# Kernel tuning notes

Hardware: AMD Instinct MI355X
Metric: run time of the kernel (lower is better)

## Reference

```python
import jax, jax.numpy as jnp
import numpy as np

BS, T, NOBJ = 16, 32, 100
GLOVE, GEMB, ADIM, GCN_DIM, H, ASPACE, RES = 300, 64, 10, 512, 512, 6, 512


def setup_inputs() -> dict:
    key = jax.random.key(0)
    ks = jax.random.split(key, 34)
    rn = lambda k, shp, s=0.02: (jax.random.normal(k, shp, jnp.float32) * s)
    inp = {}
    inp["target"] = jax.random.normal(ks[0], (BS, T, GLOVE), jnp.float32)
    inp["input_"] = jax.random.normal(ks[1], (BS, T, RES, 1, 1), jnp.float32)
    inp["action_probs"] = jax.random.uniform(ks[2], (BS, T, ASPACE), jnp.float32)
    # symmetric normalized adjacency (D^-1/2 A D^-1/2), as normalize_adj produces
    A_raw = (jax.random.uniform(ks[3], (NOBJ, NOBJ)) < 0.1).astype(jnp.float32)
    A_raw = ((A_raw + A_raw.T + jnp.eye(NOBJ)) > 0).astype(jnp.float32)
    dinv = 1.0 / jnp.sqrt(jnp.sum(A_raw, axis=1))
    inp["A"] = A_raw * dinv[:, None] * dinv[None, :]
    inp["all_glove"] = jax.random.normal(ks[4], (NOBJ, GLOVE), jnp.float32)
    inp["Wword"] = rn(ks[5], (GEMB, GLOVE)); inp["bword"] = jnp.zeros((GEMB,))
    inp["Wg"] = rn(ks[6], (GEMB, GLOVE)); inp["bg"] = jnp.zeros((GEMB,))
    inp["Wa"] = rn(ks[7], (ADIM, ASPACE)); inp["ba"] = jnp.zeros((ADIM,))
    inp["W0"] = rn(ks[8], (256, RES + GEMB))
    inp["W1"] = rn(ks[9], (256, 256))
    inp["W2"] = rn(ks[10], (1, 256))
    inp["Wfm"] = rn(ks[11], (GCN_DIM, NOBJ)); inp["bfm"] = jnp.zeros((GCN_DIM,))
    fused_in = RES + GEMB + ADIM + GCN_DIM
    inp["Wf"] = rn(ks[12], (H, fused_in)); inp["bf"] = jnp.zeros((H,))
    inp["Wih"] = rn(ks[13], (4 * H, H)); inp["Whh"] = rn(ks[14], (4 * H, H))
    inp["bih"] = jnp.zeros((4 * H,)); inp["bhh"] = jnp.zeros((4 * H,))
    inp["Wa1"] = rn(ks[15], (128, H)); inp["ba1"] = jnp.zeros((128,))
    inp["Wa2"] = rn(ks[16], (ASPACE, 128)); inp["ba2"] = jnp.zeros((ASPACE,))
    inp["Wc1"] = rn(ks[17], (128, H)); inp["bc1"] = jnp.zeros((128,))
    inp["Wc2"] = rn(ks[18], (1, 128)); inp["bc2"] = jnp.zeros((1,))
    return inp


def _forward(target, input_, action_probs, A, all_glove, Wword, bword, Wg, bg,
             Wa, ba, W0, W1, W2, Wfm, bfm, Wf, bf, Wih, Whh, bih, bhh,
             Wa1, ba1, Wa2, ba2, Wc1, bc1, Wc2, bc2):
    bs, t = target.shape[0], target.shape[1]
    B = bs * t
    feats = input_.reshape(B, RES)                      # [B,512] (squeeze 1x1)
    glove_e = jax.nn.relu(target.reshape(B, GLOVE) @ Wg.T + bg)
    act_e = jax.nn.relu(action_probs.reshape(B, ASPACE) @ Wa.T + ba)
    # GCN branch (all_glove is detached in the original)
    word = jax.lax.stop_gradient(all_glove) @ Wword.T + bword   # [N,GEMB]
    N = A.shape[0]
    class_e = jnp.broadcast_to(feats[:, None, :], (B, N, RES))
    x = jnp.concatenate([class_e, jnp.broadcast_to(word[None], (B, N, GEMB))], -1)
    x = jax.nn.relu(jnp.einsum('nm,bmd->bnd', A, x) @ W0.T)     # [B,N,256]
    x = jax.nn.relu(jnp.einsum('nm,bmd->bnd', A, x) @ W1.T)     # [B,N,256]
    x = jax.nn.relu(jnp.einsum('nm,bmd->bnd', A, x) @ W2.T)     # [B,N,1]
    gcn_e = x[..., 0] @ Wfm.T + bfm                             # [B,GCN_DIM]
    fused = jnp.concatenate([feats, glove_e, act_e, gcn_e], -1)
    out = jax.nn.relu(fused @ Wf.T + bf).reshape(bs, t, H)
    # LSTM (torch gate order i,f,g,o), batch_first, zero init state
    h0 = jnp.zeros((bs, H), out.dtype)
    c0 = jnp.zeros((bs, H), out.dtype)
    def step(carry, xt):
        h, c = carry
        g = xt @ Wih.T + h @ Whh.T + bih + bhh
        i, f, gg, o = jnp.split(g, 4, axis=-1)
        c = jax.nn.sigmoid(f) * c + jax.nn.sigmoid(i) * jnp.tanh(gg)
        h = jax.nn.sigmoid(o) * jnp.tanh(c)
        return (h, c), h
    (hT, cT), hs = jax.lax.scan(step, (h0, c0), out.transpose(1, 0, 2))
    sf = hs.transpose(1, 0, 2).reshape(B, H)
    actor = jax.nn.relu(jax.nn.relu(sf @ Wa1.T + ba1) @ Wa2.T + ba2).reshape(bs, t, ASPACE)
    critic = jax.nn.relu(jax.nn.relu(sf @ Wc1.T + bc1) @ Wc2.T + bc2).reshape(bs, t, 1)
    return actor, critic, hT[None], cT[None]


def reference(target, input_, action_probs, A, all_glove, Wword, bword, Wg, bg,
              Wa, ba, W0, W1, W2, Wfm, bfm, Wf, bf, Wih, Whh, bih, bhh,
              Wa1, ba1, Wa2, ba2, Wc1, bc1, Wc2, bc2):
    return _forward(target, input_, action_probs, A, all_glove, Wword, bword,
                    Wg, bg, Wa, ba, W0, W1, W2, Wfm, bfm, Wf, bf, Wih, Whh,
                    bih, bhh, Wa1, ba1, Wa2, ba2, Wc1, bc1, Wc2, bc2)
```

## Files before the change

kernel.cpp:

```cpp
#include <hip/hip_runtime.h>
#include <cmath>

constexpr int BSZ = 16, T = 32, NOBJ = 100;
constexpr int GLOVE = 300, GEMB = 64, ADIM = 10, GCN_DIM = 512, Hh = 512, ASPACE = 6, RES = 512;
constexpr int Bt = BSZ * T;
constexpr int FUSED_IN = RES + GEMB + ADIM + GCN_DIM;
constexpr int FP = 1120;

typedef __attribute__((ext_vector_type(8))) short bf16x8;
typedef __attribute__((ext_vector_type(4))) float f32x4;

__device__ __forceinline__ unsigned short f2bf(float f) {
    unsigned u = __float_as_uint(f);
    return (unsigned short)((u + 0x7FFFu + ((u >> 16) & 1u)) >> 16);
}
__device__ __forceinline__ unsigned pk2(float a, float b) {
    return (unsigned)f2bf(a) | ((unsigned)f2bf(b) << 16);
}
__device__ __forceinline__ float sigf(float x) { return 1.f / (1.f + __expf(-x)); }

template<bool RELU, int OMODE>
__global__ __launch_bounds__(256)
void mgemm(const unsigned short* __restrict__ A, int lda,
           const unsigned short* __restrict__ B, int ldb,
           float* __restrict__ Cf, unsigned short* __restrict__ Cb, int ldc,
           const float* __restrict__ bias, int K)
{
    const int tid = threadIdx.x;
    const int l = tid & 63, wv = tid >> 6;
    const int m0 = blockIdx.y * 64 + wv * 16;
    const int n0 = blockIdx.x * 64;
    const int lr = l & 15, kg = l >> 4;
    const unsigned short* ap = A + (long)(m0 + lr) * lda + kg * 8;
    const unsigned short* bp = B + (long)(n0 + lr) * ldb + kg * 8;
    const int nk = K >> 5;
    f32x4 acc0 = (f32x4){0.f, 0.f, 0.f, 0.f};
    f32x4 acc1 = acc0, acc2 = acc0, acc3 = acc0;
    bf16x8 a_[4], b0_[4], b1_[4], b2_[4], b3_[4];
#pragma unroll
    for (int s = 0; s < 4; ++s) {
        if (s < nk) {
            int k = s * 32;
            a_[s]  = *(const bf16x8*)(ap + k);
            b0_[s] = *(const bf16x8*)(bp + k);
            b1_[s] = *(const bf16x8*)(bp + 16 * ldb + k);
            b2_[s] = *(const bf16x8*)(bp + 32 * ldb + k);
            b3_[s] = *(const bf16x8*)(bp + 48 * ldb + k);
        }
    }
    for (int i = 0; i < nk; i += 4) {
#pragma unroll
        for (int s = 0; s < 4; ++s) {
            if (i + s < nk) {
                acc0 = __builtin_amdgcn_mfma_f32_16x16x32_bf16(a_[s], b0_[s], acc0, 0, 0, 0);
                acc1 = __builtin_amdgcn_mfma_f32_16x16x32_bf16(a_[s], b1_[s], acc1, 0, 0, 0);
                acc2 = __builtin_amdgcn_mfma_f32_16x16x32_bf16(a_[s], b2_[s], acc2, 0, 0, 0);
                acc3 = __builtin_amdgcn_mfma_f32_16x16x32_bf16(a_[s], b3_[s], acc3, 0, 0, 0);
                if (i + s + 4 < nk) {
                    int k = (i + s + 4) * 32;
                    a_[s]  = *(const bf16x8*)(ap + k);
                    b0_[s] = *(const bf16x8*)(bp + k);
                    b1_[s] = *(const bf16x8*)(bp + 16 * ldb + k);
                    b2_[s] = *(const bf16x8*)(bp + 32 * ldb + k);
                    b3_[s] = *(const bf16x8*)(bp + 48 * ldb + k);
                }
            }
        }
    }
    f32x4 av[4] = {acc0, acc1, acc2, acc3};
#pragma unroll
    for (int nf = 0; nf < 4; ++nf) {
        int n = n0 + nf * 16 + lr;
        float bs = bias ? bias[n] : 0.f;
#pragma unroll
        for (int r = 0; r < 4; ++r) {
            float val = av[nf][r] + bs;
            if (RELU) val = fmaxf(val, 0.f);
            long idx = (long)(m0 + kg * 4 + r) * ldc + n;
            if (OMODE == 0) Cf[idx] = val;
            else            Cb[idx] = f2bf(val);
        }
    }
}

template<bool RELU>
__global__ __launch_bounds__(128)
void gemm32(const float* __restrict__ A, int lda,
            const float* __restrict__ B, int ldb,
            float* __restrict__ C, int ldc,
            const float* __restrict__ bias, int M, int N, int K)
{
    __shared__ float As[32][36];
    __shared__ float Bs[32][68];
    const int tid = threadIdx.x;
    const int m0 = blockIdx.y * 32, n0 = blockIdx.x * 64;
    const int mi = tid >> 4, ni = tid & 15;
    float acc[4][4] = {};
    for (int k0 = 0; k0 < K; k0 += 32) {
        __syncthreads();
#pragma unroll
        for (int l = 0; l < 2; ++l) {
            int e = tid + l * 128;
            int row = e >> 3, kq = (e & 7) << 2;
            float4 va = make_float4(0.f, 0.f, 0.f, 0.f);
            if (m0 + row < M && k0 + kq < K)
                va = *(const float4*)&A[(long)(m0 + row) * lda + k0 + kq];
            As[kq + 0][row] = va.x; As[kq + 1][row] = va.y;
            As[kq + 2][row] = va.z; As[kq + 3][row] = va.w;
        }
#pragma unroll
        for (int l = 0; l < 4; ++l) {
            int e = tid + l * 128;
            int row = e >> 3, kq = (e & 7) << 2;
            float4 vb = make_float4(0.f, 0.f, 0.f, 0.f);
            if (n0 + row < N && k0 + kq < K)
                vb = *(const float4*)&B[(long)(n0 + row) * ldb + k0 + kq];
            Bs[kq + 0][row] = vb.x; Bs[kq + 1][row] = vb.y;
            Bs[kq + 2][row] = vb.z; Bs[kq + 3][row] = vb.w;
        }
        __syncthreads();
#pragma unroll
        for (int k = 0; k < 32; ++k) {
            float4 a4 = *(const float4*)&As[k][4 * mi];
            float4 b4 = *(const float4*)&Bs[k][4 * ni];
            acc[0][0] = fmaf(a4.x, b4.x, acc[0][0]); acc[0][1] = fmaf(a4.x, b4.y, acc[0][1]);
            acc[0][2] = fmaf(a4.x, b4.z, acc[0][2]); acc[0][3] = fmaf(a4.x, b4.w, acc[0][3]);
            acc[1][0] = fmaf(a4.y, b4.x, acc[1][0]); acc[1][1] = fmaf(a4.y, b4.y, acc[1][1]);
            acc[1][2] = fmaf(a4.y, b4.z, acc[1][2]); acc[1][3] = fmaf(a4.y, b4.w, acc[1][3]);
            acc[2][0] = fmaf(a4.z, b4.x, acc[2][0]); acc[2][1] = fmaf(a4.z, b4.y, acc[2][1]);
            acc[2][2] = fmaf(a4.z, b4.z, acc[2][2]); acc[2][3] = fmaf(a4.z, b4.w, acc[2][3]);
            acc[3][0] = fmaf(a4.w, b4.x, acc[3][0]); acc[3][1] = fmaf(a4.w, b4.y, acc[3][1]);
            acc[3][2] = fmaf(a4.w, b4.z, acc[3][2]); acc[3][3] = fmaf(a4.w, b4.w, acc[3][3]);
        }
    }
    const int n = n0 + 4 * ni;
    if (n >= N) return;
    float4 bv = make_float4(0.f, 0.f, 0.f, 0.f);
    if (bias) bv = *(const float4*)&bias[n];
#pragma unroll
    for (int r = 0; r < 4; ++r) {
        int m = m0 + 4 * mi + r;
        if (m >= M) continue;
        float4 v;
        v.x = acc[r][0] + bv.x; v.y = acc[r][1] + bv.y;
        v.z = acc[r][2] + bv.z; v.w = acc[r][3] + bv.w;
        if (RELU) {
            v.x = fmaxf(v.x, 0.f); v.y = fmaxf(v.y, 0.f);
            v.z = fmaxf(v.z, 0.f); v.w = fmaxf(v.w, 0.f);
        }
        *(float4*)&C[(long)m * ldc + n] = v;
    }
}

__global__ __launch_bounds__(256)
void x1pack(const float* __restrict__ u, const float* __restrict__ v,
            const float* __restrict__ rowsum, uint4* __restrict__ X1g)
{
    __shared__ float u_lds[256];
    __shared__ float rs_lds[112];
    const int b = blockIdx.x, tid = threadIdx.x;
    u_lds[tid] = u[(long)b * 256 + tid];
    if (tid < 112) rs_lds[tid] = (tid < 100) ? rowsum[tid] : 0.f;
    __syncthreads();
    uint4* outp = X1g + (size_t)b * 3584;
#pragma unroll
    for (int it = 0; it < 14; ++it) {
        int job = it * 256 + tid;
        int l = job & 63;
        int kt = (job >> 6) & 7;
        int mt = job >> 9;
        int n = mt * 16 + (l & 15);
        int k0 = kt * 32 + ((l >> 4) << 3);
        uint4 p = make_uint4(0, 0, 0, 0);
        if (n < 100) {
            float rsn = rs_lds[n];
            float4 u0 = *(const float4*)&u_lds[k0];
            float4 u1 = *(const float4*)&u_lds[k0 + 4];
            const float4* vp = (const float4*)&v[n * 256 + k0];
            float4 v0 = vp[0], v1 = vp[1];
            float x0 = fmaxf(fmaf(rsn, u0.x, v0.x), 0.f), x1 = fmaxf(fmaf(rsn, u0.y, v0.y), 0.f);
            float x2 = fmaxf(fmaf(rsn, u0.z, v0.z), 0.f), x3 = fmaxf(fmaf(rsn, u0.w, v0.w), 0.f);
            float x4 = fmaxf(fmaf(rsn, u1.x, v1.x), 0.f), x5 = fmaxf(fmaf(rsn, u1.y, v1.y), 0.f);
            float x6 = fmaxf(fmaf(rsn, u1.z, v1.z), 0.f), x7 = fmaxf(fmaf(rsn, u1.w, v1.w), 0.f);
            p = make_uint4(pk2(x0, x1), pk2(x2, x3), pk2(x4, x5), pk2(x6, x7));
        }
        outp[job] = p;
    }
}

constexpr int ZLD = 152;

__global__ __launch_bounds__(256, 2)
void gcn_core(const bf16x8* __restrict__ X1g,
              const float* __restrict__ Aglob,
              const bf16x8* __restrict__ W1f,
              const bf16x8* __restrict__ Af,
              const float* __restrict__ w2,
              unsigned short* __restrict__ x3b)
{
    __shared__ unsigned short Z1Ts[128 * ZLD];
    __shared__ float w2l[256];
    __shared__ float spart[4][112];
    __shared__ float sl[112];

    const int b = blockIdx.x, tid = threadIdx.x;
    const int l = tid & 63, wv = tid >> 6;
    const int lrow = l & 15, kg = l >> 4;

    w2l[tid] = w2[tid];
    if (tid < 128) {
        uint4 z = make_uint4(0, 0, 0, 0);
        *(uint4*)&Z1Ts[tid * ZLD + 112] = z;
        *(uint4*)&Z1Ts[tid * ZLD + 120] = z;
    }
    if (tid < 28) x3b[(long)b * 128 + 100 + tid] = 0;
    __syncthreads();

    const bf16x8* xb = X1g + (size_t)b * 3584 + l;

    float sacc[7][4];
#pragma unroll
    for (int mt = 0; mt < 7; ++mt)
#pragma unroll
        for (int r = 0; r < 4; ++r) sacc[mt][r] = 0.f;

    for (int half = 0; half < 2; ++half) {
        f32x4 acc1[7][2];
#pragma unroll
        for (int mt = 0; mt < 7; ++mt)
#pragma unroll
            for (int jtl = 0; jtl < 2; ++jtl) acc1[mt][jtl] = (f32x4){0.f, 0.f, 0.f, 0.f};

#pragma unroll
        for (int kt = 0; kt < 8; ++kt) {
            bf16x8 af[7];
#pragma unroll
            for (int mt = 0; mt < 7; ++mt)
                af[mt] = xb[mt * 512 + kt * 64];
#pragma unroll
            for (int jtl = 0; jtl < 2; ++jtl) {
                int jt = half * 8 + wv * 2 + jtl;
                bf16x8 bfr = W1f[(jt * 8 + kt) * 64 + l];
#pragma unroll
                for (int mt = 0; mt < 7; ++mt)
                    acc1[mt][jtl] = __builtin_amdgcn_mfma_f32_16x16x32_bf16(af[mt], bfr, acc1[mt][jtl], 0, 0, 0);
            }
        }

#pragma unroll
        for (int mt = 0; mt < 7; ++mt)
#pragma unroll
            for (int jtl = 0; jtl < 2; ++jtl) {
                int jloc = (wv * 2 + jtl) * 16 + lrow;
                f32x4 a = acc1[mt][jtl];
                uint2 zz;
                zz.x = pk2(a[0], a[1]);
                zz.y = pk2(a[2], a[3]);
                *(uint2*)&Z1Ts[jloc * ZLD + mt * 16 + kg * 4] = zz;
            }

        bf16x8 bz[2][4];
#pragma unroll
        for (int jtl = 0; jtl < 2; ++jtl)
#pragma unroll
            for (int k2 = 0; k2 < 4; ++k2)
                bz[jtl][k2] = *(const bf16x8*)&Z1Ts[((wv * 2 + jtl) * 16 + lrow) * ZLD + k2 * 32 + kg * 8];
#pragma unroll
        for (int mt = 0; mt < 7; ++mt) {
            bf16x8 aA[4];
#pragma unroll
            for (int k2 = 0; k2 < 4; ++k2) aA[k2] = Af[(mt * 4 + k2) * 64 + l];
#pragma unroll
            for (int jtl = 0; jtl < 2; ++jtl) {
                f32x4 p = (f32x4){0.f, 0.f, 0.f, 0.f};
#pragma unroll
                for (int k2 = 0; k2 < 4; ++k2)
                    p = __builtin_amdgcn_mfma_f32_16x16x32_bf16(aA[k2], bz[jtl][k2], p, 0, 0, 0);
                float w2j = w2l[half * 128 + (wv * 2 + jtl) * 16 + lrow];
#pragma unroll
                for (int r = 0; r < 4; ++r)
                    sacc[mt][r] = fmaf(fmaxf(p[r], 0.f), w2j, sacc[mt][r]);
            }
        }
    }

#pragma unroll
    for (int mt = 0; mt < 7; ++mt) {
        float s0 = sacc[mt][0], s1 = sacc[mt][1], s2 = sacc[mt][2], s3 = sacc[mt][3];
#pragma unroll
        for (int off = 1; off < 16; off <<= 1) {
            s0 += __shfl_xor(s0, off);
            s1 += __shfl_xor(s1, off);
            s2 += __shfl_xor(s2, off);
            s3 += __shfl_xor(s3, off);
        }
        if (lrow == 0) {
            int m = mt * 16 + kg * 4;
            spart[wv][m + 0] = s0; spart[wv][m + 1] = s1;
            spart[wv][m + 2] = s2; spart[wv][m + 3] = s3;
        }
    }
    __syncthreads();
    if (tid < 112)
        sl[tid] = spart[0][tid] + spart[1][tid] + spart[2][tid] + spart[3][tid];
    __syncthreads();

    float sv0 = (l < 100) ? sl[l] : 0.f;
    float sv1 = (l + 64 < 100) ? sl[l + 64] : 0.f;
#pragma unroll 5
    for (int i = 0; i < 25; ++i) {
        int n = i * 4 + wv;
        float a0 = (l < 100) ? Aglob[n * 100 + l] : 0.f;
        float a1 = (l + 64 < 100) ? Aglob[n * 100 + l + 64] : 0.f;
        float p = a0 * sv0 + a1 * sv1;
#pragma unroll
        for (int off = 32; off; off >>= 1) p += __shfl_xor(p, off);
        if (l == 0) x3b[(long)b * 128 + n] = f2bf(fmaxf(p, 0.f));
    }
}

union HU { unsigned long long u[2]; bf16x8 v; };

__global__ __launch_bounds__(256, 1)
void lstm_persist3(const float* __restrict__ xWih,
                   const bf16x8* __restrict__ Whhf,
                   unsigned long long* __restrict__ hseq,
                   unsigned* __restrict__ flags,
                   float* __restrict__ cBuf, float* __restrict__ hFin,
                   unsigned short* __restrict__ sfb)
{
    __shared__ float gl[4][16][17];
    __shared__ unsigned short htile[16][16];
    const int tid = threadIdx.x;
    const int l = tid & 63, g = tid >> 6;
    const int bid = blockIdx.x;
    const int jt = g * 32 + bid;
    const int lr = l & 15, kg = l >> 4;
    const bf16x8* wp = Whhf + (size_t)jt * 16 * 64 + l;
    bf16x8 w[16];
#pragma unroll
    for (int kt = 0; kt < 16; ++kt) w[kt] = wp[kt * 64];
    const int fb = tid >> 4, jl = tid & 15;
    const int jh = bid * 16 + jl;
    float c_reg = 0.f;
    for (int t = 0; t < T; ++t) {
        if (t > 0) {
            if (tid < 32) {
                while (__hip_atomic_load(&flags[t * 32 + tid],
                                         __ATOMIC_RELAXED, __HIP_MEMORY_SCOPE_AGENT) == 0u) { }
            }
            __syncthreads();
        }
        const unsigned long long* hp = hseq + (size_t)t * 2048 + lr * 128 + kg * 2;
        HU hu[16];
#pragma unroll
        for (int kt = 0; kt < 16; ++kt) {
            hu[kt].u[0] = __hip_atomic_load(hp + kt * 8,     __ATOMIC_RELAXED, __HIP_MEMORY_SCOPE_AGENT);
            hu[kt].u[1] = __hip_atomic_load(hp + kt * 8 + 1, __ATOMIC_RELAXED, __HIP_MEMORY_SCOPE_AGENT);
        }
        f32x4 acc = (f32x4){0.f, 0.f, 0.f, 0.f};
#pragma unroll
        for (int kt = 0; kt < 16; ++kt)
            acc = __builtin_amdgcn_mfma_f32_16x16x32_bf16(hu[kt].v, w[kt], acc, 0, 0, 0);
#pragma unroll
        for (int r = 0; r < 4; ++r) gl[g][kg * 4 + r][lr] = acc[r];
        __syncthreads();
        const float* xw = xWih + (size_t)(fb * T + t) * 2048;
        float gi = gl[0][fb][jl] + xw[jh];
        float gf = gl[1][fb][jl] + xw[512 + jh];
        float gg = gl[2][fb][jl] + xw[1024 + jh];
        float go = gl[3][fb][jl] + xw[1536 + jh];
        float cn = sigf(gf) * c_reg + sigf(gi) * tanhf(gg);
        float hn = sigf(go) * tanhf(cn);
        c_reg = cn;
        unsigned short hb = f2bf(hn);
        htile[fb][jl] = hb;
        sfb[(size_t)(fb * T + t) * 512 + jh] = hb;
        if (t == T - 1) { hFin[fb * 512 + jh] = hn; cBuf[fb * 512 + jh] = cn; }
        __syncthreads();
        if (tid < 64) {
            int row = tid >> 2, q = tid & 3;
            unsigned long long val = *(const unsigned long long*)&htile[row][q * 4];
            __hip_atomic_store(&hseq[(size_t)(t + 1) * 2048 + row * 128 + bid * 4 + q], val,
                               __ATOMIC_RELAXED, __HIP_MEMORY_SCOPE_AGENT);
        }
        __syncthreads();
        if (tid == 0)
            __hip_atomic_store(&flags[(t + 1) * 32 + bid], 1u,
                               __ATOMIC_RELAXED, __HIP_MEMORY_SCOPE_AGENT);
    }
}

__global__ void k_aw_rowsum(const float* __restrict__ A, const float* __restrict__ word,
                            float* __restrict__ Aw, float* __restrict__ rowsum)
{
    int i = blockIdx.x * 256 + threadIdx.x;
    if (i < 6400) {
        int n = i / 64, k = i % 64;
        float s = 0.f;
        for (int m = 0; m < 100; ++m) s += A[n * 100 + m] * word[m * 64 + k];
        Aw[i] = s;
    } else if (i < 6500) {
        int n = i - 6400;
        float s = 0.f;
        for (int m = 0; m < 100; ++m) s += A[n * 100 + m];
        rowsum[n] = s;
    }
}

__global__ void k_prep(const float* __restrict__ Whh, uint4* __restrict__ Whhf,
                       const float* __restrict__ Wf, unsigned short* __restrict__ WfPb,
                       const float* __restrict__ Wih, unsigned short* __restrict__ Wihb,
                       const float* __restrict__ Wa1, const float* __restrict__ Wc1,
                       unsigned short* __restrict__ Whdb,
                       const float* __restrict__ ba1, const float* __restrict__ bc1,
                       float* __restrict__ bhd,
                       const float* __restrict__ Wg, unsigned short* __restrict__ Wgb,
                       const float* __restrict__ W0, unsigned short* __restrict__ W0ab,
                       const float* __restrict__ Wfm, unsigned short* __restrict__ Wfmb,
                       const float* __restrict__ target, unsigned short* __restrict__ tgtb,
                       const float* __restrict__ feats, unsigned short* __restrict__ featsb,
                       unsigned short* __restrict__ fusedb,
                       const float* __restrict__ aprob, const float* __restrict__ Wa,
                       const float* __restrict__ ba,
                       unsigned short* __restrict__ h0s, unsigned* __restrict__ flags,
                       const float* __restrict__ bih, const float* __restrict__ bhh,
                       float* __restrict__ bsum,
                       const float* __restrict__ W1, uint4* __restrict__ W1f,
                       const float* __restrict__ A, uint4* __restrict__ Af)
{
    int bx = blockIdx.x, tid = threadIdx.x;
    if (bx < 512) {
        int job = bx * 256 + tid;
        int jtkt = job >> 6, ll = job & 63;
        int j = (jtkt >> 4) * 16 + (ll & 15);
        int k0 = (jtkt & 15) * 32 + (ll >> 4) * 8;
        const float* src = &Whh[(long)j * 512 + k0];
        uint4 p;
        p.x = pk2(src[0], src[1]); p.y = pk2(src[2], src[3]);
        p.z = pk2(src[4], src[5]); p.w = pk2(src[6], src[7]);
        Whhf[job] = p;
    } else if (bx < 2752) {
        int i = (bx - 512) * 256 + tid;
        int r = i / FP, c = i - r * FP;
        WfPb[i] = f2bf(c < FUSED_IN ? Wf[(long)r * FUSED_IN + c] : 0.f);
    } else if (bx < 6848) {
        int i = (bx - 2752) * 256 + tid;
        Wihb[i] = f2bf(Wih[i]);
    } else if (bx < 7360) {
        int i = (bx - 6848) * 256 + tid;
        int r = i >> 9, c = i & 511;
        Whdb[i] = f2bf(r < 128 ? Wa1[r * 512 + c] : Wc1[(r - 128) * 512 + c]);
    } else if (bx < 7361) {
        bhd[tid] = (tid < 128) ? ba1[tid] : bc1[tid - 128];
    } else if (bx < 7441) {
        int i = (bx - 7361) * 256 + tid;
        int r = i / 320, c = i - r * 320;
        Wgb[i] = f2bf(c < GLOVE ? Wg[r * GLOVE + c] : 0.f);
    } else if (bx < 7953) {
        int i = (bx - 7441) * 256 + tid;
        int r = i >> 9, c = i & 511;
        W0ab[i] = f2bf(W0[(long)r * 576 + c]);
    } else if (bx < 8209) {
        int i = (bx - 7953) * 256 + tid;
        int r = i >> 7, c = i & 127;
        Wfmb[i] = f2bf(c < 100 ? Wfm[r * 100 + c] : 0.f);
    } else if (bx < 8849) {
        int i = (bx - 8209) * 256 + tid;
        int r = i / 320, c = i - r * 320;
        tgtb[i] = f2bf(c < GLOVE ? target[(long)r * GLOVE + c] : 0.f);
    } else if (bx < 9873) {
        int i = (bx - 8849) * 256 + tid;
        featsb[i] = f2bf(feats[i]);
    } else if (bx < 10897) {
        int i = (bx - 9873) * 256 + tid;
        int r = i >> 9, c = i & 511;
        fusedb[(long)r * FP + c] = f2bf(feats[i]);
    } else if (bx < 10917) {
        int i = (bx - 10897) * 256 + tid;
        int r = i / 10, c6 = i - r * 10;
        float s = ba[c6];
#pragma unroll
        for (int k = 0; k < 6; ++k) s += aprob[r * 6 + k] * Wa[c6 * 6 + k];
        fusedb[(long)r * FP + 576 + c6] = f2bf(fmaxf(s, 0.f));
    } else if (bx < 10961) {
        int i = (bx - 10917) * 256 + tid;
        int r = i / 22, c = 1098 + (i - r * 22);
        fusedb[(long)r * FP + c] = 0;
    } else if (bx < 10993) {
        int i = (bx - 10961) * 256 + tid;
        h0s[i] = 0;
    } else if (bx < 10998) {
        int i = (bx - 10993) * 256 + tid;
        if (i < (T + 1) * 32) flags[i] = 0u;
    } else if (bx < 11006) {
        int i = (bx - 10998) * 256 + tid;
        bsum[i] = bih[i] + bhh[i];
    } else if (bx < 11038) {
        int job = (bx - 11006) * 256 + tid;
        int jt = job >> 9, rem = job & 511, kt = rem >> 6, lane = rem & 63;
        int j = jt * 16 + (lane & 15), k0 = kt * 32 + (lane >> 4) * 8;
        const float* src = &W1[(long)j * 256 + k0];
        uint4 p;
        p.x = pk2(src[0], src[1]); p.y = pk2(src[2], src[3]);
        p.z = pk2(src[4], src[5]); p.w = pk2(src[6], src[7]);
        W1f[job] = p;
    } else {
        int job = (bx - 11038) * 256 + tid;
        int mt = job >> 8, rem = job & 255, kt = rem >> 6, lane = rem & 63;
        int m = mt * 16 + (lane & 15), n0 = kt * 32 + (lane >> 4) * 8;
        float h[8];
#pragma unroll
        for (int e = 0; e < 8; ++e)
            h[e] = (m < 100 && n0 + e < 100) ? A[m * 100 + n0 + e] : 0.f;
        uint4 p;
        p.x = pk2(h[0], h[1]); p.y = pk2(h[2], h[3]);
        p.z = pk2(h[4], h[5]); p.w = pk2(h[6], h[7]);
        Af[job] = p;
    }
}

__global__ void k_finish(const float* __restrict__ hd,
                         const float* __restrict__ Wa2, const float* __restrict__ ba2,
                         const float* __restrict__ Wc2, const float* __restrict__ bc2,
                         const float* __restrict__ hFin, const float* __restrict__ cBuf,
                         float* __restrict__ out)
{
    if (blockIdx.x < 32) {
        int row = blockIdx.x * 16 + (threadIdx.x >> 4);
        int slot = threadIdx.x & 15;
        if (slot < 6) {
            const float4* h4 = (const float4*)(hd + (long)row * 256);
            const float4* w4 = (const float4*)(Wa2 + slot * 128);
            float s = 0.f;
#pragma unroll
            for (int k = 0; k < 32; ++k) {
                float4 h = h4[k], w = w4[k];
                s += h.x * w.x + h.y * w.y + h.z * w.z + h.w * w.w;
            }
            out[row * 6 + slot] = fmaxf(s + ba2[slot], 0.f);
        } else if (slot == 6) {
            const float4* h4 = (const float4*)(hd + (long)row * 256 + 128);
            const float4* w4 = (const float4*)(Wc2);
            float s = 0.f;
#pragma unroll
            for (int k = 0; k < 32; ++k) {
                float4 h = h4[k], w = w4[k];
                s += h.x * w.x + h.y * w.y + h.z * w.z + h.w * w.w;
            }
            out[3072 + row] = fmaxf(s + bc2[0], 0.f);
        }
    } else {
        int i = (blockIdx.x - 32) * 256 + threadIdx.x;
        out[3584 + i] = hFin[i];
        out[11776 + i] = cBuf[i];
    }
}

static inline void mg(hipStream_t st, const unsigned short* A, int lda,
                      const unsigned short* B, int ldb,
                      float* Cf, unsigned short* Cb, int ldc,
                      const float* bias, int M, int N, int K, bool relu, bool bf16out)
{
    dim3 g(N / 64, M / 64), blk(256);
    if (bf16out) {
        if (relu) hipLaunchKernelGGL((mgemm<true, 1>), g, blk, 0, st, A, lda, B, ldb, Cf, Cb, ldc, bias, K);
        else      hipLaunchKernelGGL((mgemm<false, 1>), g, blk, 0, st, A, lda, B, ldb, Cf, Cb, ldc, bias, K);
    } else {
        if (relu) hipLaunchKernelGGL((mgemm<true, 0>), g, blk, 0, st, A, lda, B, ldb, Cf, Cb, ldc, bias, K);
        else      hipLaunchKernelGGL((mgemm<false, 0>), g, blk, 0, st, A, lda, B, ldb, Cf, Cb, ldc, bias, K);
    }
}
static inline void g32(hipStream_t st, const float* A, int lda, const float* B, int ldb,
                       float* C, int ldc, const float* bias, int M, int N, int K, bool relu)
{
    dim3 g((N + 63) / 64, (M + 31) / 32), blk(128);
    if (relu) hipLaunchKernelGGL((gemm32<true>), g, blk, 0, st, A, lda, B, ldb, C, ldc, bias, M, N, K);
    else      hipLaunchKernelGGL((gemm32<false>), g, blk, 0, st, A, lda, B, ldb, C, ldc, bias, M, N, K);
}

extern "C" void kernel_launch(void* const* d_in, const int* in_sizes, int n_in,
                              void* d_out, int out_size, void* d_ws, size_t ws_size,
                              hipStream_t stream)
{
    const float* target = (const float*)d_in[0];
    const float* input_ = (const float*)d_in[1];
    const float* aprob  = (const float*)d_in[2];
    const float* Adj    = (const float*)d_in[3];
    const float* aglove = (const float*)d_in[4];
    const float* Wword  = (const float*)d_in[5];
    const float* bword  = (const float*)d_in[6];
    const float* Wg     = (const float*)d_in[7];
    const float* bg     = (const float*)d_in[8];
    const float* Wa     = (const float*)d_in[9];
    const float* ba     = (const float*)d_in[10];
    const float* W0     = (const float*)d_in[11];
    const float* W1     = (const float*)d_in[12];
    const float* W2     = (const float*)d_in[13];
    const float* Wfm    = (const float*)d_in[14];
    const float* bfm    = (const float*)d_in[15];
    const float* Wf     = (const float*)d_in[16];
    const float* bf     = (const float*)d_in[17];
    const float* Wih    = (const float*)d_in[18];
    const float* Whh    = (const float*)d_in[19];
    const float* bih    = (const float*)d_in[20];
    const float* bhh    = (const float*)d_in[21];
    const float* Wa1    = (const float*)d_in[22];
    const float* ba1    = (const float*)d_in[23];
    const float* Wa2    = (const float*)d_in[24];
    const float* ba2    = (const float*)d_in[25];
    const float* Wc1    = (const float*)d_in[26];
    const float* bc1    = (const float*)d_in[27];
    const float* Wc2    = (const float*)d_in[28];
    const float* bc2    = (const float*)d_in[29];

    float* ws = (float*)d_ws;
    float* out = (float*)d_out;

    size_t off = 0;
    auto alloc = [&](size_t n) { size_t r = off; off += (n + 255) & ~(size_t)255; return r; };
    float* u       = ws + alloc(512 * 256);
    float* word    = ws + alloc(100 * 64);
    float* Aw      = ws + alloc(100 * 64);
    float* rowsum  = ws + alloc(128);
    float* v       = ws + alloc(100 * 256);
    float* bsum    = ws + alloc(2048);
    float* bhd     = ws + alloc(256);
    float* xWih    = ws + alloc((size_t)512 * 2048);
    float* hd      = ws + alloc(512 * 256);
    float* hFin    = ws + alloc(BSZ * Hh);
    float* cBuf    = ws + alloc(BSZ * Hh);
    float* W1frag  = ws + alloc(32768);
    float* Afrag   = ws + alloc(7168);
    float* Whhf    = ws + alloc((size_t)524288);
    float* X1gf    = ws + alloc((size_t)512 * 3584 * 4);
    float* hseqf   = ws + alloc((size_t)(T + 1) * 2048 * 2);
    unsigned* flags = (unsigned*)(ws + alloc(2048));
    unsigned short* x3b     = (unsigned short*)(ws + alloc(512 * 128 / 2));
    unsigned short* fusedb  = (unsigned short*)(ws + alloc((size_t)512 * FP / 2));
    unsigned short* WfPb    = (unsigned short*)(ws + alloc((size_t)512 * FP / 2));
    unsigned short* outfb   = (unsigned short*)(ws + alloc(512 * 512 / 2));
    unsigned short* Wihb    = (unsigned short*)(ws + alloc((size_t)2048 * 512 / 2));
    unsigned short* Whdb    = (unsigned short*)(ws + alloc(256 * 512 / 2));
    unsigned short* Wgb     = (unsigned short*)(ws + alloc(64 * 320 / 2));
    unsigned short* W0ab    = (unsigned short*)(ws + alloc(256 * 512 / 2));
    unsigned short* Wfmb    = (unsigned short*)(ws + alloc(512 * 128 / 2));
    unsigned short* tgtb    = (unsigned short*)(ws + alloc(512 * 320 / 2));
    unsigned short* featsb  = (unsigned short*)(ws + alloc(512 * 512 / 2));
    unsigned short* sfb     = (unsigned short*)(ws + alloc(512 * 512 / 2));
    (void)ws_size; (void)in_sizes; (void)n_in; (void)out_size;

    const float* feats = input_;

    hipLaunchKernelGGL(k_prep, dim3(11045), dim3(256), 0, stream,
                       Whh, (uint4*)Whhf, Wf, WfPb, Wih, Wihb, Wa1, Wc1, Whdb, ba1, bc1, bhd,
                       Wg, Wgb, W0, W0ab, Wfm, Wfmb, target, tgtb, feats, featsb,
                       fusedb, aprob, Wa, ba,
                       (unsigned short*)hseqf, flags, bih, bhh, bsum,
                       W1, (uint4*)W1frag, Adj, (uint4*)Afrag);

    g32(stream, aglove, GLOVE, Wword, GLOVE, word, 64, bword, 100, 64, GLOVE, false);
    hipLaunchKernelGGL(k_aw_rowsum, dim3(26), dim3(256), 0, stream, Adj, word, Aw, rowsum);
    g32(stream, Aw, 64, W0 + 512, 576, v, 256, nullptr, 100, 256, 64, false);

    mg(stream, featsb, 512, W0ab, 512, u, nullptr, 256, nullptr, 512, 256, 512, false, false);
    mg(stream, tgtb, 320, Wgb, 320, nullptr, fusedb + 512, FP, bg, 512, 64, 320, true, true);

    hipLaunchKernelGGL(x1pack, dim3(Bt), dim3(256), 0, stream, u, v, rowsum, (uint4*)X1gf);
    hipLaunchKernelGGL(gcn_core, dim3(Bt), dim3(256), 0, stream,
                       (const bf16x8*)X1gf, Adj, (const bf16x8*)W1frag, (const bf16x8*)Afrag, W2, x3b);
    mg(stream, x3b, 128, Wfmb, 128, nullptr, fusedb + 586, FP, bfm, 512, 512, 128, false, true);

    mg(stream, fusedb, FP, WfPb, FP, nullptr, outfb, 512, bf, 512, 512, FP, true, true);
    mg(stream, outfb, 512, Wihb, 512, xWih, nullptr, 2048, bsum, 512, 2048, 512, false, false);

    hipLaunchKernelGGL(lstm_persist3, dim3(32), dim3(256), 0, stream,
                       xWih, (const bf16x8*)Whhf,
                       (unsigned long long*)hseqf, flags, cBuf, hFin, sfb);

    mg(stream, sfb, 512, Whdb, 512, hd, nullptr, 256, bhd, 512, 256, 512, true, false);
    hipLaunchKernelGGL(k_finish, dim3(64), dim3(256), 0, stream,
                       hd, Wa2, ba2, Wc2, bc2, hFin, cBuf, out);
}
```

Baseline: 377.0 us.

## Replace LSTM per-step flag barrier with data-embedded sentinel polling on hidden state

The persistent LSTM kernel no longer waits on per-block flags followed by a block barrier. Each thread now polls its own 64-bit hidden-state words directly until they become nonzero, using zero as a sentinel. A computed zero word is replaced by 1, which alters those bf16 values slightly. The prep kernel now zeroes the hidden-sequence buffer for steps 1 and later, and step 0 skips the recurrent matmul because h0 is zero. This removes the flag store, two syncthreads per step, and a serialized handshake, at the cost of more polling traffic.

```diff
diff --git a/kernel.cpp b/kernel.cpp
--- a/kernel.cpp
+++ b/kernel.cpp
@@ -322,10 +322,9 @@
 union HU { unsigned long long u[2]; bf16x8 v; };
 
 __global__ __launch_bounds__(256, 1)
-void lstm_persist3(const float* __restrict__ xWih,
+void lstm_persist4(const float* __restrict__ xWih,
                    const bf16x8* __restrict__ Whhf,
                    unsigned long long* __restrict__ hseq,
-                   unsigned* __restrict__ flags,
                    float* __restrict__ cBuf, float* __restrict__ hFin,
                    unsigned short* __restrict__ sfb)
 {
@@ -344,24 +343,29 @@
     const int jh = bid * 16 + jl;
     float c_reg = 0.f;
     for (int t = 0; t < T; ++t) {
+        f32x4 acc = (f32x4){0.f, 0.f, 0.f, 0.f};
         if (t > 0) {
-            if (tid < 32) {
-                while (__hip_atomic_load(&flags[t * 32 + tid],
-                                         __ATOMIC_RELAXED, __HIP_MEMORY_SCOPE_AGENT) == 0u) { }
-            }
-            __syncthreads();
-        }
-        const unsigned long long* hp = hseq + (size_t)t * 2048 + lr * 128 + kg * 2;
-        HU hu[16];
-#pragma unroll
-        for (int kt = 0; kt < 16; ++kt) {
-            hu[kt].u[0] = __hip_atomic_load(hp + kt * 8,     __ATOMIC_RELAXED, __HIP_MEMORY_SCOPE_AGENT);
-            hu[kt].u[1] = __hip_atomic_load(hp + kt * 8 + 1, __ATOMIC_RELAXED, __HIP_MEMORY_SCOPE_AGENT);
-        }
-        f32x4 acc = (f32x4){0.f, 0.f, 0.f, 0.f};
-#pragma unroll
-        for (int kt = 0; kt < 16; ++kt)
-            acc = __builtin_amdgcn_mfma_f32_16x16x32_bf16(hu[kt].v, w[kt], acc, 0, 0, 0);
+            const unsigned long long* hp = hseq + (size_t)t * 2048 + lr * 128 + kg * 2;
+            unsigned long long hv[32];
+#pragma unroll
+            for (int kt = 0; kt < 16; ++kt) {
+                hv[2 * kt]     = __hip_atomic_load(hp + kt * 8,     __ATOMIC_RELAXED, __HIP_MEMORY_SCOPE_AGENT);
+                hv[2 * kt + 1] = __hip_atomic_load(hp + kt * 8 + 1, __ATOMIC_RELAXED, __HIP_MEMORY_SCOPE_AGENT);
+            }
+#pragma unroll
+            for (int q = 0; q < 32; ++q) {
+                while (hv[q] == 0ull)
+                    hv[q] = __hip_atomic_load(hp + (q >> 1) * 8 + (q & 1),
+                                              __ATOMIC_RELAXED, __HIP_MEMORY_SCOPE_AGENT);
+            }
+#pragma unroll
+            for (int kt = 0; kt < 16; ++kt) {
+                HU hu;
+                hu.u[0] = hv[2 * kt];
+                hu.u[1] = hv[2 * kt + 1];
+                acc = __builtin_amdgcn_mfma_f32_16x16x32_bf16(hu.v, w[kt], acc, 0, 0, 0);
+            }
+        }
 #pragma unroll
         for (int r = 0; r < 4; ++r) gl[g][kg * 4 + r][lr] = acc[r];
         __syncthreads();
@@ -381,13 +385,10 @@
         if (tid < 64) {
             int row = tid >> 2, q = tid & 3;
             unsigned long long val = *(const unsigned long long*)&htile[row][q * 4];
+            if (val == 0ull) val = 1ull;
             __hip_atomic_store(&hseq[(size_t)(t + 1) * 2048 + row * 128 + bid * 4 + q], val,
                                __ATOMIC_RELAXED, __HIP_MEMORY_SCOPE_AGENT);
         }
-        __syncthreads();
-        if (tid == 0)
-            __hip_atomic_store(&flags[(t + 1) * 32 + bid], 1u,
-                               __ATOMIC_RELAXED, __HIP_MEMORY_SCOPE_AGENT);
     }
 }
 
@@ -423,7 +424,7 @@
                        unsigned short* __restrict__ fusedb,
                        const float* __restrict__ aprob, const float* __restrict__ Wa,
                        const float* __restrict__ ba,
-                       unsigned short* __restrict__ h0s, unsigned* __restrict__ flags,
+                       unsigned long long* __restrict__ hz,
                        const float* __restrict__ bih, const float* __restrict__ bhh,
                        float* __restrict__ bsum,
                        const float* __restrict__ W1, uint4* __restrict__ W1f,
@@ -487,17 +488,14 @@
         int i = (bx - 10917) * 256 + tid;
         int r = i / 22, c = 1098 + (i - r * 22);
         fusedb[(long)r * FP + c] = 0;
-    } else if (bx < 10993) {
+    } else if (bx < 11217) {
         int i = (bx - 10961) * 256 + tid;
-        h0s[i] = 0;
-    } else if (bx < 10998) {
-        int i = (bx - 10993) * 256 + tid;
-        if (i < (T + 1) * 32) flags[i] = 0u;
-    } else if (bx < 11006) {
-        int i = (bx - 10998) * 256 + tid;
+        __hip_atomic_store(&hz[2048 + i], 0ull, __ATOMIC_RELAXED, __HIP_MEMORY_SCOPE_AGENT);
+    } else if (bx < 11225) {
+        int i = (bx - 11217) * 256 + tid;
         bsum[i] = bih[i] + bhh[i];
-    } else if (bx < 11038) {
-        int job = (bx - 11006) * 256 + tid;
+    } else if (bx < 11257) {
+        int job = (bx - 11225) * 256 + tid;
         int jt = job >> 9, rem = job & 511, kt = rem >> 6, lane = rem & 63;
         int j = jt * 16 + (lane & 15), k0 = kt * 32 + (lane >> 4) * 8;
         const float* src = &W1[(long)j * 256 + k0];
@@ -506,7 +504,7 @@
         p.z = pk2(src[4], src[5]); p.w = pk2(src[6], src[7]);
         W1f[job] = p;
     } else {
-        int job = (bx - 11038) * 256 + tid;
+        int job = (bx - 11257) * 256 + tid;
         int mt = job >> 8, rem = job & 255, kt = rem >> 6, lane = rem & 63;
         int m = mt * 16 + (lane & 15), n0 = kt * 32 + (lane >> 4) * 8;
         float h[8];
@@ -635,7 +633,6 @@
     float* Whhf    = ws + alloc((size_t)524288);
     float* X1gf    = ws + alloc((size_t)512 * 3584 * 4);
     float* hseqf   = ws + alloc((size_t)(T + 1) * 2048 * 2);
-    unsigned* flags = (unsigned*)(ws + alloc(2048));
     unsigned short* x3b     = (unsigned short*)(ws + alloc(512 * 128 / 2));
     unsigned short* fusedb  = (unsigned short*)(ws + alloc((size_t)512 * FP / 2));
     unsigned short* WfPb    = (unsigned short*)(ws + alloc((size_t)512 * FP / 2));
@@ -652,11 +649,11 @@
 
     const float* feats = input_;
 
-    hipLaunchKernelGGL(k_prep, dim3(11045), dim3(256), 0, stream,
+    hipLaunchKernelGGL(k_prep, dim3(11264), dim3(256), 0, stream,
                        Whh, (uint4*)Whhf, Wf, WfPb, Wih, Wihb, Wa1, Wc1, Whdb, ba1, bc1, bhd,
                        Wg, Wgb, W0, W0ab, Wfm, Wfmb, target, tgtb, feats, featsb,
                        fusedb, aprob, Wa, ba,
-                       (unsigned short*)hseqf, flags, bih, bhh, bsum,
+                       (unsigned long long*)hseqf, bih, bhh, bsum,
                        W1, (uint4*)W1frag, Adj, (uint4*)Afrag);
 
     g32(stream, aglove, GLOVE, Wword, GLOVE, word, 64, bword, 100, 64, GLOVE, false);
@@ -674,9 +671,9 @@
     mg(stream, fusedb, FP, WfPb, FP, nullptr, outfb, 512, bf, 512, 512, FP, true, true);
     mg(stream, outfb, 512, Wihb, 512, xWih, nullptr, 2048, bsum, 512, 2048, 512, false, false);
 
-    hipLaunchKernelGGL(lstm_persist3, dim3(32), dim3(256), 0, stream,
+    hipLaunchKernelGGL(lstm_persist4, dim3(32), dim3(256), 0, stream,
                        xWih, (const bf16x8*)Whhf,
-                       (unsigned long long*)hseqf, flags, cBuf, hFin, sfb);
+                       (unsigned long long*)hseqf, cBuf, hFin, sfb);
 
     mg(stream, sfb, 512, Whdb, 512, hd, nullptr, 256, bhd, 512, 256, 512, true, false);
     hipLaunchKernelGGL(k_finish, dim3(64), dim3(256), 0, stream,
```

After: 447.7 us. +18.8%, slower.
